# Kernel tuning notes

Hardware: AMD Instinct MI355X
Metric: run time of the kernel (lower is better)

## Reference

```python
import jax, jax.numpy as jnp
import numpy as np

N_SPINS = 64
BATCH = 1_000_000
N_COUPLINGS = N_SPINS * (N_SPINS - 1) // 2  # 2016


def setup_inputs() -> dict:
    key = jax.random.key(0)
    k1, k2, k3 = jax.random.split(key, 3)
    # Ising spins are +/-1; sample random +/-1 states (Bernoulli(0.5) mapped to {-1,+1})
    states = jnp.where(jax.random.bernoulli(k1, 0.5, (BATCH, N_SPINS)), 1.0, -1.0).astype(jnp.float32)
    couplings_sigma = 1.0 / N_SPINS
    couplings = (jax.random.normal(k2, (N_COUPLINGS,), dtype=jnp.float32) * couplings_sigma)
    fields = (jax.random.normal(k3, (N_SPINS,), dtype=jnp.float32) * (1.0 / couplings_sigma))
    return {"states": states, "couplings": couplings, "fields": fields}


def _coupling_matrix(couplings, n):
    # scatter lower-diagonal coupling vector into [n,n] matrix and symmetrize
    rows, cols = jnp.tril_indices(n, k=-1)
    M = jnp.zeros((n, n), dtype=couplings.dtype).at[rows, cols].set(couplings)
    return M + M.T


def reference(states, couplings, fields) -> jnp.ndarray:
    n = fields.shape[0]
    J = _coupling_matrix(couplings, n)            # [N, N] symmetric, zero diagonal
    # H_couplings[b] = s_b^T J s_b ; H_fields[b] = f . s_b
    Js = states @ J                               # [B, N]
    H_couplings = jnp.einsum("bi,bi->b", states, Js)
    H_fields = states @ fields                    # [B]
    return -H_couplings - H_fields
```

## Files before the change

kernel.cpp:

```cpp
#include <hip/hip_runtime.h>

#define NSPIN   64
#define BATCH_N 1000000
#define NTILES  (BATCH_N / 16)
#define NBLOCKS 3125
#define NWAVES  (NBLOCKS * 4)
#define TPW     (NTILES / NWAVES)

typedef __bf16 bf16x8 __attribute__((ext_vector_type(8)));
typedef float  f32x4  __attribute__((ext_vector_type(4)));

__device__ __forceinline__ unsigned fbits(float x) {
    union { float f; unsigned u; } cv; cv.f = x; return cv.u;
}
__device__ __forceinline__ unsigned pack2(float lo, float hi) {
    return __builtin_amdgcn_perm(fbits(hi), fbits(lo), 0x07060302u);
}

__device__ __forceinline__ void gload_lds16(const void* g, void* l) {
    __builtin_amdgcn_global_load_lds(
        (const __attribute__((address_space(1))) unsigned int*)g,
        (__attribute__((address_space(3))) unsigned int*)l, 16, 0, 0);
}

__global__ __launch_bounds__(256, 4) void ham_kernel(
    const float* __restrict__ states,
    const float* __restrict__ couplings,
    const float* __restrict__ fields,
    float* __restrict__ out)
{
    __shared__ char smem[32 * 1024];

    {
        __bf16* J = (__bf16*)smem;
        for (int i = threadIdx.x; i < NSPIN * NSPIN; i += 256) {
            int r = i >> 6, c = i & 63;
            float v = 0.0f;
            if (r > c)      v = couplings[(r * (r - 1)) / 2 + c];
            else if (r < c) v = couplings[(c * (c - 1)) / 2 + r];
            J[i] = (__bf16)v;
        }
    }
    __syncthreads();

    const int lane = threadIdx.x & 63;
    const int wid  = threadIdx.x >> 6;
    const int lo16 = lane & 15;
    const int g4   = lane >> 4;
    const int gw   = blockIdx.x * 4 + wid;

    bf16x8 jf[4][2];
    {
        const __bf16* J = (const __bf16*)smem;
#pragma unroll
        for (int nb = 0; nb < 4; ++nb)
#pragma unroll
            for (int kb = 0; kb < 2; ++kb)
                jf[nb][kb] = *(const bf16x8*)(J + (nb * 16 + lo16) * NSPIN + kb * 32 + g4 * 8);
    }
    f32x4 ffrag[4];
#pragma unroll
    for (int nb = 0; nb < 4; ++nb)
        ffrag[nb] = *(const f32x4*)(fields + nb * 16 + g4 * 4);

    __syncthreads();

    char* mybuf = smem + wid * 8192;

    int srcoff[4];
#pragma unroll
    for (int j = 0; j < 4; ++j) {
        int row   = 4 * j + (lane >> 4);
        int chunk = (lane & 15) ^ (row & 7);
        srcoff[j] = row * 256 + chunk * 16;
    }

    const char* sbase = (const char*)states;
    auto stage = [&](int buf, int t) {
        const char* src = sbase + (size_t)t * 4096;
#pragma unroll
        for (int j = 0; j < 4; ++j)
            gload_lds16(src + srcoff[j], mybuf + buf * 4096 + j * 1024);
    };
    auto lds_at = [&](const char* B, int row, int c) -> const void* {
        return (const void*)(B + row * 256 + (c ^ ((row & 7) << 4)));
    };

    stage(0, gw);

#pragma unroll
    for (int i = 0; i < TPW; ++i) {
        const int t = gw + i * NWAVES;
        if (i + 1 < TPW) {
            stage((i + 1) & 1, t + NWAVES);
            asm volatile("s_waitcnt vmcnt(4)" ::: "memory");
        } else {
            asm volatile("s_waitcnt vmcnt(0)" ::: "memory");
        }
        __builtin_amdgcn_sched_barrier(0);

        const char* B = mybuf + (i & 1) * 4096;

        f32x4 a0 = *(const f32x4*)lds_at(B, lo16, g4 * 32);
        f32x4 a1 = *(const f32x4*)lds_at(B, lo16, g4 * 32 + 16);
        f32x4 a2 = *(const f32x4*)lds_at(B, lo16, 128 + g4 * 32);
        f32x4 a3 = *(const f32x4*)lds_at(B, lo16, 128 + g4 * 32 + 16);

        f32x4 rv[4];
#pragma unroll
        for (int nb = 0; nb < 4; ++nb)
            rv[nb] = *(const f32x4*)lds_at(B, lo16, nb * 64 + g4 * 16);

        union { bf16x8 v; unsigned u[4]; } af0, af1;
        af0.u[0] = pack2(a0[0], a0[1]);
        af0.u[1] = pack2(a0[2], a0[3]);
        af0.u[2] = pack2(a1[0], a1[1]);
        af0.u[3] = pack2(a1[2], a1[3]);
        af1.u[0] = pack2(a2[0], a2[1]);
        af1.u[1] = pack2(a2[2], a2[3]);
        af1.u[2] = pack2(a3[0], a3[1]);
        af1.u[3] = pack2(a3[2], a3[3]);

        f32x4 acc[4];
#pragma unroll
        for (int nb = 0; nb < 4; ++nb) acc[nb] = ffrag[nb];
#pragma unroll
        for (int nb = 0; nb < 4; ++nb) {
            acc[nb] = __builtin_amdgcn_mfma_f32_16x16x32_bf16(jf[nb][0], af0.v, acc[nb], 0, 0, 0);
            acc[nb] = __builtin_amdgcn_mfma_f32_16x16x32_bf16(jf[nb][1], af1.v, acc[nb], 0, 0, 0);
        }

        float p = 0.f;
#pragma unroll
        for (int nb = 0; nb < 4; ++nb) {
            p += rv[nb][0] * acc[nb][0];
            p += rv[nb][1] * acc[nb][1];
            p += rv[nb][2] * acc[nb][2];
            p += rv[nb][3] * acc[nb][3];
        }
        p += __shfl_xor(p, 16, 64);
        p += __shfl_xor(p, 32, 64);
        if (g4 == 0)
            out[t * 16 + lo16] = -p;
    }
}

extern "C" void kernel_launch(void* const* d_in, const int* in_sizes, int n_in,
                              void* d_out, int out_size, void* d_ws, size_t ws_size,
                              hipStream_t stream) {
    const float* states    = (const float*)d_in[0];
    const float* couplings = (const float*)d_in[1];
    const float* fields    = (const float*)d_in[2];
    float* out = (float*)d_out;
    ham_kernel<<<NBLOCKS, 256, 0, stream>>>(states, couplings, fields, out);
}
```

Before: 50.20 us.

## Prebuild J in workspace and deepen states prefetch to triple buffering

A small kernel now builds the bf16 coupling matrix once in the workspace, so each block reads its J fragments from global memory instead of rebuilding J in LDS and paying two barriers. The per-wave states staging moves from double to triple buffering, with two tiles in flight, to hide more global-load latency. LDS per block grows from 32 KB to 48 KB, which can lower the number of resident blocks per CU. The extra kernel launch adds a small fixed cost.

```diff
diff --git a/kernel.cpp b/kernel.cpp
--- a/kernel.cpp
+++ b/kernel.cpp
@@ -9,6 +9,17 @@
 
 typedef __bf16 bf16x8 __attribute__((ext_vector_type(8)));
 typedef float  f32x4  __attribute__((ext_vector_type(4)));
+
+__global__ void build_J_kernel(const float* __restrict__ couplings,
+                               __bf16* __restrict__ Jg) {
+    int idx = blockIdx.x * blockDim.x + threadIdx.x;
+    if (idx >= NSPIN * NSPIN) return;
+    int r = idx >> 6, c = idx & 63;
+    float v = 0.0f;
+    if (r > c)      v = couplings[(r * (r - 1)) / 2 + c];
+    else if (r < c) v = couplings[(c * (c - 1)) / 2 + r];
+    Jg[idx] = (__bf16)v;
+}
 
 __device__ __forceinline__ unsigned fbits(float x) {
     union { float f; unsigned u; } cv; cv.f = x; return cv.u;
@@ -23,15 +34,30 @@
         (__attribute__((address_space(3))) unsigned int*)l, 16, 0, 0);
 }
 
+template<bool USE_WS>
 __global__ __launch_bounds__(256, 4) void ham_kernel(
     const float* __restrict__ states,
     const float* __restrict__ couplings,
     const float* __restrict__ fields,
+    const __bf16* __restrict__ Jg,
     float* __restrict__ out)
 {
-    __shared__ char smem[32 * 1024];
+    __shared__ char smem[48 * 1024];
 
-    {
+    const int lane = threadIdx.x & 63;
+    const int wid  = threadIdx.x >> 6;
+    const int lo16 = lane & 15;
+    const int g4   = lane >> 4;
+    const int gw   = blockIdx.x * 4 + wid;
+
+    bf16x8 jf[4][2];
+    if constexpr (USE_WS) {
+#pragma unroll
+        for (int nb = 0; nb < 4; ++nb)
+#pragma unroll
+            for (int kb = 0; kb < 2; ++kb)
+                jf[nb][kb] = *(const bf16x8*)(Jg + (nb * 16 + lo16) * NSPIN + kb * 32 + g4 * 8);
+    } else {
         __bf16* J = (__bf16*)smem;
         for (int i = threadIdx.x; i < NSPIN * NSPIN; i += 256) {
             int r = i >> 6, c = i & 63;
@@ -40,38 +66,27 @@
             else if (r < c) v = couplings[(c * (c - 1)) / 2 + r];
             J[i] = (__bf16)v;
         }
-    }
-    __syncthreads();
-
-    const int lane = threadIdx.x & 63;
-    const int wid  = threadIdx.x >> 6;
-    const int lo16 = lane & 15;
-    const int g4   = lane >> 4;
-    const int gw   = blockIdx.x * 4 + wid;
-
-    bf16x8 jf[4][2];
-    {
-        const __bf16* J = (const __bf16*)smem;
+        __syncthreads();
 #pragma unroll
         for (int nb = 0; nb < 4; ++nb)
 #pragma unroll
             for (int kb = 0; kb < 2; ++kb)
                 jf[nb][kb] = *(const bf16x8*)(J + (nb * 16 + lo16) * NSPIN + kb * 32 + g4 * 8);
+        __syncthreads();
     }
+
     f32x4 ffrag[4];
 #pragma unroll
     for (int nb = 0; nb < 4; ++nb)
         ffrag[nb] = *(const f32x4*)(fields + nb * 16 + g4 * 4);
 
-    __syncthreads();
-
-    char* mybuf = smem + wid * 8192;
+    char* mybuf = smem + wid * (3 * 4096);
 
     int srcoff[4];
 #pragma unroll
     for (int j = 0; j < 4; ++j) {
-        int row   = 4 * j + (lane >> 4);
-        int chunk = (lane & 15) ^ (row & 7);
+        int row   = 4 * j + g4;
+        int chunk = lo16 ^ (row & 7);
         srcoff[j] = row * 256 + chunk * 16;
     }
 
@@ -87,19 +102,22 @@
     };
 
     stage(0, gw);
+    stage(1, gw + NWAVES);
 
 #pragma unroll
     for (int i = 0; i < TPW; ++i) {
         const int t = gw + i * NWAVES;
-        if (i + 1 < TPW) {
-            stage((i + 1) & 1, t + NWAVES);
+        if (i + 2 < TPW) {
+            stage((i + 2) % 3, t + 2 * NWAVES);
+            asm volatile("s_waitcnt vmcnt(8)" ::: "memory");
+        } else if (i + 2 == TPW) {
             asm volatile("s_waitcnt vmcnt(4)" ::: "memory");
         } else {
             asm volatile("s_waitcnt vmcnt(0)" ::: "memory");
         }
         __builtin_amdgcn_sched_barrier(0);
 
-        const char* B = mybuf + (i & 1) * 4096;
+        const char* B = mybuf + (i % 3) * 4096;
 
         f32x4 a0 = *(const f32x4*)lds_at(B, lo16, g4 * 32);
         f32x4 a1 = *(const f32x4*)lds_at(B, lo16, g4 * 32 + 16);
@@ -152,5 +170,12 @@
     const float* couplings = (const float*)d_in[1];
     const float* fields    = (const float*)d_in[2];
     float* out = (float*)d_out;
-    ham_kernel<<<NBLOCKS, 256, 0, stream>>>(states, couplings, fields, out);
+
+    if (ws_size >= NSPIN * NSPIN * sizeof(__bf16)) {
+        __bf16* Jg = (__bf16*)d_ws;
+        build_J_kernel<<<16, 256, 0, stream>>>(couplings, Jg);
+        ham_kernel<true><<<NBLOCKS, 256, 0, stream>>>(states, couplings, fields, Jg, out);
+    } else {
+        ham_kernel<false><<<NBLOCKS, 256, 0, stream>>>(states, couplings, fields, nullptr, out);
+    }
 }
```

Result: faster. 47.13 us (-6.1%).

## Replace LDS double-buffered async staging with direct global vector loads

Applied to the files above, without the earlier changes.

Removes the global_load_lds double-buffered staging of state tiles through swizzled shared memory. Each lane now reads its state row fragments straight from global memory with 16-byte vector loads, and shared memory shrinks to the 8KB J matrix. This drops the LDS round trip, the explicit vmcnt waits and the second barrier, and may raise occupancy. In exchange there is no explicit prefetch overlap, the state data is loaded twice per lane (the MFMA operand and the rv values) unless the cache catches it, and the per-lane access pattern may coalesce less well.

```diff
diff --git a/kernel.cpp b/kernel.cpp
--- a/kernel.cpp
+++ b/kernel.cpp
@@ -5,7 +5,6 @@
 #define NTILES  (BATCH_N / 16)
 #define NBLOCKS 3125
 #define NWAVES  (NBLOCKS * 4)
-#define TPW     (NTILES / NWAVES)
 
 typedef __bf16 bf16x8 __attribute__((ext_vector_type(8)));
 typedef float  f32x4  __attribute__((ext_vector_type(4)));
@@ -17,99 +16,52 @@
     return __builtin_amdgcn_perm(fbits(hi), fbits(lo), 0x07060302u);
 }
 
-__device__ __forceinline__ void gload_lds16(const void* g, void* l) {
-    __builtin_amdgcn_global_load_lds(
-        (const __attribute__((address_space(1))) unsigned int*)g,
-        (__attribute__((address_space(3))) unsigned int*)l, 16, 0, 0);
-}
-
 __global__ __launch_bounds__(256, 4) void ham_kernel(
     const float* __restrict__ states,
     const float* __restrict__ couplings,
     const float* __restrict__ fields,
     float* __restrict__ out)
 {
-    __shared__ char smem[32 * 1024];
-
-    {
-        __bf16* J = (__bf16*)smem;
-        for (int i = threadIdx.x; i < NSPIN * NSPIN; i += 256) {
-            int r = i >> 6, c = i & 63;
-            float v = 0.0f;
-            if (r > c)      v = couplings[(r * (r - 1)) / 2 + c];
-            else if (r < c) v = couplings[(c * (c - 1)) / 2 + r];
-            J[i] = (__bf16)v;
-        }
-    }
-    __syncthreads();
-
     const int lane = threadIdx.x & 63;
     const int wid  = threadIdx.x >> 6;
     const int lo16 = lane & 15;
     const int g4   = lane >> 4;
     const int gw   = blockIdx.x * 4 + wid;
 
+    __shared__ __bf16 J[NSPIN * NSPIN];
+    for (int i = threadIdx.x; i < NSPIN * NSPIN; i += 256) {
+        int r = i >> 6, c = i & 63;
+        float v = 0.0f;
+        if (r > c)      v = couplings[(r * (r - 1)) / 2 + c];
+        else if (r < c) v = couplings[(c * (c - 1)) / 2 + r];
+        J[i] = (__bf16)v;
+    }
+    __syncthreads();
+
     bf16x8 jf[4][2];
-    {
-        const __bf16* J = (const __bf16*)smem;
 #pragma unroll
-        for (int nb = 0; nb < 4; ++nb)
+    for (int nb = 0; nb < 4; ++nb)
 #pragma unroll
-            for (int kb = 0; kb < 2; ++kb)
-                jf[nb][kb] = *(const bf16x8*)(J + (nb * 16 + lo16) * NSPIN + kb * 32 + g4 * 8);
-    }
+        for (int kb = 0; kb < 2; ++kb)
+            jf[nb][kb] = *(const bf16x8*)(J + (nb * 16 + lo16) * NSPIN + kb * 32 + g4 * 8);
+
     f32x4 ffrag[4];
 #pragma unroll
     for (int nb = 0; nb < 4; ++nb)
         ffrag[nb] = *(const f32x4*)(fields + nb * 16 + g4 * 4);
 
-    __syncthreads();
+    for (int t = gw; t < NTILES; t += NWAVES) {
+        const float* row = states + (size_t)t * (16 * NSPIN) + lo16 * NSPIN;
 
-    char* mybuf = smem + wid * 8192;
-
-    int srcoff[4];
-#pragma unroll
-    for (int j = 0; j < 4; ++j) {
-        int row   = 4 * j + (lane >> 4);
-        int chunk = (lane & 15) ^ (row & 7);
-        srcoff[j] = row * 256 + chunk * 16;
-    }
-
-    const char* sbase = (const char*)states;
-    auto stage = [&](int buf, int t) {
-        const char* src = sbase + (size_t)t * 4096;
-#pragma unroll
-        for (int j = 0; j < 4; ++j)
-            gload_lds16(src + srcoff[j], mybuf + buf * 4096 + j * 1024);
-    };
-    auto lds_at = [&](const char* B, int row, int c) -> const void* {
-        return (const void*)(B + row * 256 + (c ^ ((row & 7) << 4)));
-    };
-
-    stage(0, gw);
-
-#pragma unroll
-    for (int i = 0; i < TPW; ++i) {
-        const int t = gw + i * NWAVES;
-        if (i + 1 < TPW) {
-            stage((i + 1) & 1, t + NWAVES);
-            asm volatile("s_waitcnt vmcnt(4)" ::: "memory");
-        } else {
-            asm volatile("s_waitcnt vmcnt(0)" ::: "memory");
-        }
-        __builtin_amdgcn_sched_barrier(0);
-
-        const char* B = mybuf + (i & 1) * 4096;
-
-        f32x4 a0 = *(const f32x4*)lds_at(B, lo16, g4 * 32);
-        f32x4 a1 = *(const f32x4*)lds_at(B, lo16, g4 * 32 + 16);
-        f32x4 a2 = *(const f32x4*)lds_at(B, lo16, 128 + g4 * 32);
-        f32x4 a3 = *(const f32x4*)lds_at(B, lo16, 128 + g4 * 32 + 16);
+        f32x4 a0 = *(const f32x4*)(row + g4 * 8);
+        f32x4 a1 = *(const f32x4*)(row + g4 * 8 + 4);
+        f32x4 a2 = *(const f32x4*)(row + 32 + g4 * 8);
+        f32x4 a3 = *(const f32x4*)(row + 32 + g4 * 8 + 4);
 
         f32x4 rv[4];
 #pragma unroll
         for (int nb = 0; nb < 4; ++nb)
-            rv[nb] = *(const f32x4*)lds_at(B, lo16, nb * 64 + g4 * 16);
+            rv[nb] = *(const f32x4*)(row + nb * 16 + g4 * 4);
 
         union { bf16x8 v; unsigned u[4]; } af0, af1;
         af0.u[0] = pack2(a0[0], a0[1]);
```

After: 73.44 us. 1.46x slower.
